# Optimization experiments

Hardware: AMD Instinct MI355X
Metric: run time of the kernel (lower is better)

## Reference

```python
import jax, jax.numpy as jnp
import numpy as np
import math

B, L, D, H = 2, 2048, 1024, 16
DK = D // H  # 64


def _lin(k, din, dout):
    kw, kb = jax.random.split(k)
    w = jax.random.normal(kw, (din, dout), dtype=jnp.float32) * 0.02
    b = jax.random.normal(kb, (dout,), dtype=jnp.float32) * 0.02
    return w, b


def setup_inputs() -> dict:
    key = jax.random.key(0)
    ks = jax.random.split(key, 12)
    wq, bq = _lin(ks[0], D, D)
    wk, bk = _lin(ks[1], D, D)
    wv, bv = _lin(ks[2], D, D)
    wo, bo = _lin(ks[3], D, D)
    whq, bhq = _lin(ks[4], DK, DK)
    whk, bhk = _lin(ks[5], DK, DK)
    whv, bhv = _lin(ks[6], DK, DK)
    who, bho = _lin(ks[7], DK, DK)
    return {
        "q_input": jax.random.normal(ks[8], (B, L, D), dtype=jnp.float32),
        "k_input": jax.random.normal(ks[9], (B, L, D), dtype=jnp.float32),
        "v_input": jax.random.normal(ks[10], (B, L, D), dtype=jnp.float32),
        "mask": jnp.ones((B, 1, L, L), dtype=jnp.int32),
        "wq": wq, "bq": bq, "wk": wk, "bk": bk, "wv": wv, "bv": bv,
        "wo": wo, "bo": bo,
        "whq": whq, "bhq": bhq, "whk": whk, "bhk": bhk,
        "whv": whv, "bhv": bhv, "who": who, "bho": bho,
    }


def reference(q_input, k_input, v_input, mask, wq, bq, wk, bk, wv, bv, wo, bo,
              whq, bhq, whk, bhk, whv, bhv, who, bho):
    scale = 1.0 / math.sqrt(DK)
    # Q/K/V projections -> [B, H, L, DK]
    Q = (q_input @ wq + bq).reshape(B, L, H, DK).transpose(0, 2, 1, 3)
    K = (k_input @ wk + bk).reshape(B, L, H, DK).transpose(0, 2, 1, 3)
    V = (v_input @ wv + bv).reshape(B, L, H, DK).transpose(0, 2, 1, 3)
    scores = jnp.einsum('bhqd,bhkd->bhqk', Q, K) * scale  # [B,H,L,L]
    neg = jnp.finfo(scores.dtype).min
    scores = jnp.where(mask == 0, neg, scores)
    probs = jax.nn.softmax(scores, axis=-1)  # dropout is identity in eval
    attn = jnp.einsum('bhqk,bhkd->bhqd', probs, V)
    heads = attn.transpose(0, 2, 1, 3)  # [B, L, H, DK]
    # Inter-head attention over the head dimension (size H) per position
    Qh = heads @ whq + bhq
    Kh = heads @ whk + bhk
    Vh = heads @ whv + bhv
    inter = jnp.einsum('blhd,blgd->blhg', Qh, Kh) * scale  # [B,L,H,H]
    iprobs = jax.nn.softmax(inter, axis=-1)
    mixed = jnp.einsum('blhg,blgd->blhd', iprobs, Vh)  # [B,L,H,DK]
    # note: inter_head_out is defined but unused in the original forward
    concat = mixed.reshape(B, L, D)
    return concat @ wo + bo
```

## Files before the change

kernel.cpp:

```cpp
#include <hip/hip_runtime.h>
#include <hip/hip_bf16.h>

typedef __bf16 bf16_t;
typedef __bf16 bf16x4 __attribute__((ext_vector_type(4)));
typedef __bf16 bf16x8 __attribute__((ext_vector_type(8)));
typedef float f32x4 __attribute__((ext_vector_type(4)));

typedef __attribute__((address_space(1))) unsigned char glob_u8;
typedef __attribute__((address_space(3))) unsigned char lds_u8;

__device__ __forceinline__ void load_lds16(const void* g, void* l) {
    __builtin_amdgcn_global_load_lds((glob_u8*)g, (lds_u8*)l, 16, 0, 0);
}

__global__ void prep1_kernel(const int* __restrict__ mask, int* __restrict__ flags,
                             const float* __restrict__ wq, const float* __restrict__ wk,
                             const float* __restrict__ wv, bf16_t* __restrict__ wqkvT,
                             const float* __restrict__ aq, const float* __restrict__ ak,
                             const float* __restrict__ av, bf16_t* __restrict__ abf)
{
    const int bid = blockIdx.x, t = threadIdx.x;
    if (bid < 2048) {
        int b = bid >> 10, qt = (bid >> 5) & 31, kt = bid & 31;
        int ok = 1;
#pragma unroll
        for (int i = 0; i < 16; i++) {
            int e = t + i * 256; int r = e >> 6, c = e & 63;
            ok &= (mask[((size_t)b * 2048 + qt * 64 + r) * 2048 + kt * 64 + c] != 0) ? 1 : 0;
        }
        ok = __syncthreads_and(ok);
        if (t == 0) flags[bid] = ok;
    } else if (bid < 2816) {
        __shared__ bf16_t tile[64][65];
        int idx = bid - 2048;
        int z = idx >> 8, rem = idx & 255;
        const float* src = (z == 0) ? wq : (z == 1) ? wk : wv;
        bf16_t* dst = wqkvT + (size_t)z * 1048576;
        int rB = (rem >> 4) * 64, cB = (rem & 15) * 64;
#pragma unroll
        for (int i = 0; i < 16; i++) {
            int e = t + i * 256; int r = e >> 6, c = e & 63;
            tile[r][c] = (bf16_t)src[(size_t)(rB + r) * 1024 + cB + c];
        }
        __syncthreads();
#pragma unroll
        for (int i = 0; i < 16; i++) {
            int e = t + i * 256; int r = e >> 6, c = e & 63;
            dst[(size_t)(cB + r) * 1024 + rB + c] = tile[c][r];
        }
    } else {
        int idx = bid - 2816;
        int z = idx >> 9, seg = idx & 511;
        const float* src = (z == 0) ? aq : (z == 1) ? ak : av;
        bf16_t* dst = abf + (size_t)z * 4194304;
        size_t base = (size_t)seg * 8192 + (size_t)t * 32;
#pragma unroll
        for (int j = 0; j < 4; j++) {
            f32x4 u = *(const f32x4*)(src + base + j * 8);
            f32x4 v = *(const f32x4*)(src + base + j * 8 + 4);
            bf16x8 o;
            o[0] = (bf16_t)u[0]; o[1] = (bf16_t)u[1];
            o[2] = (bf16_t)u[2]; o[3] = (bf16_t)u[3];
            o[4] = (bf16_t)v[0]; o[5] = (bf16_t)v[1];
            o[6] = (bf16_t)v[2]; o[7] = (bf16_t)v[3];
            *(bf16x8*)(dst + base + j * 8) = o;
        }
    }
}

__global__ void prep2_kernel(const float* __restrict__ wo, bf16_t* __restrict__ woT,
                             const float* __restrict__ s0, const float* __restrict__ s1,
                             const float* __restrict__ s2,
                             bf16_t* __restrict__ d0, bf16_t* __restrict__ d1, bf16_t* __restrict__ d2)
{
    const int bid = blockIdx.x, t = threadIdx.x;
    if (bid < 256) {
        __shared__ bf16_t tile[64][65];
        int rB = (bid >> 4) * 64, cB = (bid & 15) * 64;
#pragma unroll
        for (int i = 0; i < 16; i++) {
            int e = t + i * 256; int r = e >> 6, c = e & 63;
            tile[r][c] = (bf16_t)wo[(size_t)(rB + r) * 1024 + cB + c];
        }
        __syncthreads();
#pragma unroll
        for (int i = 0; i < 16; i++) {
            int e = t + i * 256; int r = e >> 6, c = e & 63;
            woT[(size_t)(cB + r) * 1024 + rB + c] = tile[c][r];
        }
    } else {
        int z = bid - 256;
        const float* src = (z == 0) ? s0 : (z == 1) ? s1 : s2;
        bf16_t* dst = (z == 0) ? d0 : (z == 1) ? d1 : d2;
#pragma unroll
        for (int i = 0; i < 16; i++) {
            int e = t + i * 256; int r = e >> 6, c = e & 63;
            dst[c * 64 + r] = (bf16_t)src[r * 64 + c];
        }
    }
}

#define GS 40

template<bool BF16A>
__global__ __launch_bounds__(256, 2) void gemm_qkv_t(
    const float* __restrict__ Aq, const float* __restrict__ Ak, const float* __restrict__ Av,
    const bf16_t* __restrict__ Abf,
    const bf16_t* __restrict__ WT,
    const float* __restrict__ bq, const float* __restrict__ bk, const float* __restrict__ bv,
    bf16_t* __restrict__ outbase)
{
    __shared__ bf16_t As[128 * GS];
    __shared__ bf16_t Bs[128 * GS];
    const int z = blockIdx.z;
    const float* A    = (z == 0) ? Aq : (z == 1) ? Ak : Av;
    const bf16_t* Ab  = Abf + (size_t)z * 4194304;
    const bf16_t* Bt  = WT + (size_t)z * 1048576;
    const float* bia  = (z == 0) ? bq : (z == 1) ? bk : bv;
    bf16_t* out = outbase + (size_t)z * 4194304;

    const int t = threadIdx.x;
    const int w = t >> 6, lane = t & 63;
    const int lane15 = lane & 15, quad = lane >> 4;
    const int wr = w >> 1, wc = w & 1;
    const int rowBase = blockIdx.x * 128, colBase = blockIdx.y * 128;

    const int ar = t >> 1, ac = (t & 1) * 16;
    const int e0 = t * 8, e1 = (256 + t) * 8;
    const int r0 = e0 >> 5, c0 = e0 & 31;
    const int r1 = e1 >> 5, c1 = e1 & 31;

    f32x4 acc[4][4];
    f32x4 zf = {0.f, 0.f, 0.f, 0.f};
#pragma unroll
    for (int i = 0; i < 4; i++)
#pragma unroll
        for (int j = 0; j < 4; j++) acc[i][j] = zf;

    for (int k0 = 0; k0 < 1024; k0 += 32) {
        bf16x8 av0, av1;
        if (BF16A) {
            const bf16_t* ab = Ab + (size_t)(rowBase + ar) * 1024 + k0 + ac;
            av0 = *(const bf16x8*)(ab);
            av1 = *(const bf16x8*)(ab + 8);
        } else {
            const float4* ap = (const float4*)(A + (size_t)(rowBase + ar) * 1024 + k0 + ac);
            float4 af4[4];
#pragma unroll
            for (int i = 0; i < 4; i++) af4[i] = ap[i];
#pragma unroll
            for (int i = 0; i < 4; i++) {
                bf16x8& dstv = (i < 2) ? av0 : av1;
                int base = (i & 1) * 4;
                dstv[base + 0] = (bf16_t)af4[i].x; dstv[base + 1] = (bf16_t)af4[i].y;
                dstv[base + 2] = (bf16_t)af4[i].z; dstv[base + 3] = (bf16_t)af4[i].w;
            }
        }
        bf16x8 b0 = *(const bf16x8*)(Bt + (size_t)(colBase + r0) * 1024 + k0 + c0);
        bf16x8 b1 = *(const bf16x8*)(Bt + (size_t)(colBase + r1) * 1024 + k0 + c1);
        *(bf16x8*)(As + ar * GS + ac) = av0;
        *(bf16x8*)(As + ar * GS + ac + 8) = av1;
        *(bf16x8*)(Bs + r0 * GS + c0) = b0;
        *(bf16x8*)(Bs + r1 * GS + c1) = b1;
        __syncthreads();
        bf16x8 afr[4], bfr[4];
#pragma unroll
        for (int mi = 0; mi < 4; mi++)
            afr[mi] = *(const bf16x8*)(As + (wr * 64 + mi * 16 + lane15) * GS + quad * 8);
#pragma unroll
        for (int ni = 0; ni < 4; ni++)
            bfr[ni] = *(const bf16x8*)(Bs + (wc * 64 + ni * 16 + lane15) * GS + quad * 8);
#pragma unroll
        for (int mi = 0; mi < 4; mi++)
#pragma unroll
            for (int ni = 0; ni < 4; ni++)
                acc[mi][ni] = __builtin_amdgcn_mfma_f32_16x16x32_bf16(afr[mi], bfr[ni], acc[mi][ni], 0, 0, 0);
        __syncthreads();
    }

#pragma unroll
    for (int ni = 0; ni < 4; ni++) {
        int col = colBase + wc * 64 + ni * 16 + lane15;
        float bias = bia[col];
        int h = col >> 6, dk = col & 63;
#pragma unroll
        for (int mi = 0; mi < 4; mi++) {
#pragma unroll
            for (int r = 0; r < 4; r++) {
                int row = rowBase + wr * 64 + mi * 16 + quad * 4 + r;
                int b = row >> 11, l = row & 2047;
                float v = acc[mi][ni][r] + bias;
                size_t dst = (z < 2) ? ((((size_t)(b * 16 + h)) * 2048 + l) * 64 + dk)
                                     : ((((size_t)(b * 16 + h)) * 64 + dk) * 2048 + l);
                out[dst] = (bf16_t)v;
            }
        }
    }
}

__global__ __launch_bounds__(256, 2) void gemm_out_kernel(
    const bf16_t* __restrict__ A, const bf16_t* __restrict__ Bt,
    const float* __restrict__ bia, float* __restrict__ out)
{
    __shared__ bf16_t As[128 * 32];
    __shared__ bf16_t Bs[64 * 32];
    const int t = threadIdx.x;
    const int w = t >> 6, lane = t & 63;
    const int lane15 = lane & 15, quad = lane >> 4;
    const int wr = w >> 1, wc = w & 1;
    const int rowBase = blockIdx.x * 128, colBase = blockIdx.y * 64;

    const int brow = lane >> 2, bcol = (lane & 3) * 8;

    f32x4 acc[4][2];
    f32x4 zf = {0.f, 0.f, 0.f, 0.f};
#pragma unroll
    for (int i = 0; i < 4; i++)
#pragma unroll
        for (int j = 0; j < 2; j++) acc[i][j] = zf;

    for (int k0 = 0; k0 < 1024; k0 += 32) {
#pragma unroll
        for (int j = 0; j < 2; j++) {
            int chunk = w * 2 + j;
            load_lds16(A + (size_t)(rowBase + chunk * 16 + brow) * 1024 + k0 + bcol,
                       (char*)As + chunk * 1024);
        }
        {
            int chunk = w;
            load_lds16(Bt + (size_t)(colBase + chunk * 16 + brow) * 1024 + k0 + bcol,
                       (char*)Bs + chunk * 1024);
        }
        __syncthreads();
        bf16x8 afr[4], bfr[2];
#pragma unroll
        for (int mi = 0; mi < 4; mi++)
            afr[mi] = *(const bf16x8*)(As + (wr * 64 + mi * 16 + lane15) * 32 + quad * 8);
#pragma unroll
        for (int ni = 0; ni < 2; ni++)
            bfr[ni] = *(const bf16x8*)(Bs + (wc * 32 + ni * 16 + lane15) * 32 + quad * 8);
#pragma unroll
        for (int mi = 0; mi < 4; mi++)
#pragma unroll
            for (int ni = 0; ni < 2; ni++)
                acc[mi][ni] = __builtin_amdgcn_mfma_f32_16x16x32_bf16(afr[mi], bfr[ni], acc[mi][ni], 0, 0, 0);
        __syncthreads();
    }

#pragma unroll
    for (int ni = 0; ni < 2; ni++) {
        int col = colBase + wc * 32 + ni * 16 + lane15;
        float bias = bia[col];
#pragma unroll
        for (int mi = 0; mi < 4; mi++) {
#pragma unroll
            for (int r = 0; r < 4; r++) {
                int row = rowBase + wr * 64 + mi * 16 + quad * 4 + r;
                out[(size_t)row * 1024 + col] = acc[mi][ni][r] + bias;
            }
        }
    }
}

#define FS 72

__global__ __launch_bounds__(256, 4) void flash_kernel(
    const bf16_t* __restrict__ QKV, const int* __restrict__ mask,
    const int* __restrict__ flags, bf16_t* __restrict__ attnout)
{
    __shared__ bf16_t Ks[64 * FS];
    __shared__ bf16_t Vs[64 * FS];
    __shared__ bf16_t Ps[8 * 16 * FS];
    const int t = threadIdx.x, w = t >> 6, lane = t & 63;
    const int lane15 = lane & 15, quad = lane >> 4;
    const int qt = blockIdx.y, bh = blockIdx.x;
    const int b = bh >> 4, h = bh & 15;
    const bf16_t* Q  = QKV;
    const bf16_t* K  = QKV + 4194304;
    const bf16_t* Vt = QKV + 8388608;
    const int qrow0 = qt * 128 + w * 32;

    bf16x8 aq[2][2];
#pragma unroll
    for (int qf = 0; qf < 2; qf++) {
        const bf16_t* qb = Q + ((size_t)bh * 2048 + qrow0 + qf * 16 + lane15) * 64;
        aq[qf][0] = *(const bf16x8*)(qb + quad * 8);
        aq[qf][1] = *(const bf16x8*)(qb + 32 + quad * 8);
#pragma unroll
        for (int j = 0; j < 8; j++) {
            aq[qf][0][j] = (bf16_t)((float)aq[qf][0][j] * 0.125f);
            aq[qf][1][j] = (bf16_t)((float)aq[qf][1][j] * 0.125f);
        }
    }

    f32x4 zf = {0.f, 0.f, 0.f, 0.f};
    f32x4 o[2][4];
#pragma unroll
    for (int qf = 0; qf < 2; qf++)
#pragma unroll
        for (int df = 0; df < 4; df++) o[qf][df] = zf;
    f32x4 lsum[2] = {zf, zf};
    bf16_t* Pw0 = Ps + (w * 2 + 0) * 16 * FS;
    bf16_t* Pw1 = Ps + (w * 2 + 1) * 16 * FS;
    bf16x8 ones;
#pragma unroll
    for (int j = 0; j < 8; j++) ones[j] = (bf16_t)1.0f;

    const int e0 = t * 8, e1 = (256 + t) * 8;
    const int kr0 = e0 >> 6, kc0 = e0 & 63, kr1 = e1 >> 6, kc1 = e1 & 63;
    const int* flagrow = flags + (b * 32 + qt) * 32;
    const bf16_t* Kb  = K  + (size_t)bh * 131072;
    const bf16_t* Vtb = Vt + (size_t)bh * 131072;

    {
        bf16x8 k0v = *(const bf16x8*)(Kb  + (size_t)kr0 * 64 + kc0);
        bf16x8 k1v = *(const bf16x8*)(Kb  + (size_t)kr1 * 64 + kc1);
        bf16x8 v0v = *(const bf16x8*)(Vtb + (size_t)kr0 * 2048 + kc0);
        bf16x8 v1v = *(const bf16x8*)(Vtb + (size_t)kr1 * 2048 + kc1);
        *(bf16x8*)(Ks + kr0 * FS + kc0) = k0v;
        *(bf16x8*)(Ks + kr1 * FS + kc1) = k1v;
        *(bf16x8*)(Vs + kr0 * FS + kc0) = v0v;
        *(bf16x8*)(Vs + kr1 * FS + kc1) = v1v;
    }
    __syncthreads();

    for (int kt = 0; kt < 32; kt++) {
        bf16x8 k0v, k1v, v0v, v1v;
        if (kt + 1 < 32) {
            int kn = (kt + 1) * 64;
            k0v = *(const bf16x8*)(Kb  + (size_t)(kn + kr0) * 64 + kc0);
            k1v = *(const bf16x8*)(Kb  + (size_t)(kn + kr1) * 64 + kc1);
            v0v = *(const bf16x8*)(Vtb + (size_t)kr0 * 2048 + kn + kc0);
            v1v = *(const bf16x8*)(Vtb + (size_t)kr1 * 2048 + kn + kc1);
        }

        f32x4 st[2][4];
#pragma unroll
        for (int kf = 0; kf < 4; kf++) {
            bf16x8 kb0 = *(const bf16x8*)(Ks + (kf * 16 + lane15) * FS + quad * 8);
            bf16x8 kb1 = *(const bf16x8*)(Ks + (kf * 16 + lane15) * FS + 32 + quad * 8);
#pragma unroll
            for (int qf = 0; qf < 2; qf++) {
                f32x4 a = zf;
                a = __builtin_amdgcn_mfma_f32_16x16x32_bf16(kb0, aq[qf][0], a, 0, 0, 0);
                a = __builtin_amdgcn_mfma_f32_16x16x32_bf16(kb1, aq[qf][1], a, 0, 0, 0);
                st[qf][kf] = a * 1.44269504f;
            }
        }
        if (!flagrow[kt]) {
#pragma unroll
            for (int qf = 0; qf < 2; qf++)
#pragma unroll
                for (int kf = 0; kf < 4; kf++)
#pragma unroll
                    for (int r = 0; r < 4; r++) {
                        int qrow = qrow0 + qf * 16 + lane15;
                        int kpos = kt * 64 + kf * 16 + quad * 4 + r;
                        if (mask[((size_t)b * 2048 + qrow) * 2048 + kpos] == 0)
                            st[qf][kf][r] = -1e30f;
                    }
        }
#pragma unroll
        for (int qf = 0; qf < 2; qf++) {
            bf16_t* Pq = qf ? Pw1 : Pw0;
#pragma unroll
            for (int kf = 0; kf < 4; kf++) {
                bf16x4 pv;
#pragma unroll
                for (int r = 0; r < 4; r++) pv[r] = (bf16_t)exp2f(st[qf][kf][r]);
                *(bf16x4*)(Pq + lane15 * FS + kf * 16 + quad * 4) = pv;
            }
        }
        bf16x8 pa[2][2];
        pa[0][0] = *(const bf16x8*)(Pw0 + lane15 * FS + quad * 8);
        pa[0][1] = *(const bf16x8*)(Pw0 + lane15 * FS + 32 + quad * 8);
        pa[1][0] = *(const bf16x8*)(Pw1 + lane15 * FS + quad * 8);
        pa[1][1] = *(const bf16x8*)(Pw1 + lane15 * FS + 32 + quad * 8);
#pragma unroll
        for (int qf = 0; qf < 2; qf++) {
            lsum[qf] = __builtin_amdgcn_mfma_f32_16x16x32_bf16(ones, pa[qf][0], lsum[qf], 0, 0, 0);
            lsum[qf] = __builtin_amdgcn_mfma_f32_16x16x32_bf16(ones, pa[qf][1], lsum[qf], 0, 0, 0);
        }
#pragma unroll
        for (int df = 0; df < 4; df++) {
            bf16x8 vb0 = *(const bf16x8*)(Vs + (df * 16 + lane15) * FS + quad * 8);
            bf16x8 vb1 = *(const bf16x8*)(Vs + (df * 16 + lane15) * FS + 32 + quad * 8);
#pragma unroll
            for (int qf = 0; qf < 2; qf++) {
                o[qf][df] = __builtin_amdgcn_mfma_f32_16x16x32_bf16(pa[qf][0], vb0, o[qf][df], 0, 0, 0);
                o[qf][df] = __builtin_amdgcn_mfma_f32_16x16x32_bf16(pa[qf][1], vb1, o[qf][df], 0, 0, 0);
            }
        }

        if (kt + 1 < 32) {
            __syncthreads();
            *(bf16x8*)(Ks + kr0 * FS + kc0) = k0v;
            *(bf16x8*)(Ks + kr1 * FS + kc1) = k1v;
            *(bf16x8*)(Vs + kr0 * FS + kc0) = v0v;
            *(bf16x8*)(Vs + kr1 * FS + kc1) = v1v;
            __syncthreads();
        }
    }

#pragma unroll
    for (int qf = 0; qf < 2; qf++) {
        float lv = lsum[qf][0];
#pragma unroll
        for (int r = 0; r < 4; r++) {
            float inv = 1.0f / __shfl(lv, quad * 4 + r, 64);
            size_t row = (size_t)b * 2048 + qrow0 + qf * 16 + quad * 4 + r;
#pragma unroll
            for (int df = 0; df < 4; df++)
                attnout[(row * 16 + h) * 64 + df * 16 + lane15] = (bf16_t)(o[qf][df][r] * inv);
        }
    }
}

__global__ __launch_bounds__(256, 2) void interhead_kernel(
    const bf16_t* __restrict__ attn,
    const bf16_t* __restrict__ whqT, const float* __restrict__ bhq,
    const bf16_t* __restrict__ whkT, const float* __restrict__ bhk,
    const bf16_t* __restrict__ whvT, const float* __restrict__ bhv,
    bf16_t* __restrict__ concat)
{
    __shared__ bf16_t lds[4 * 4608];
    const int t = threadIdx.x, w = t >> 6, lane = t & 63;
    const int lane15 = lane & 15, quad = lane >> 4;
    bf16_t* Qh  = lds + w * 4608;
    bf16_t* Kh  = Qh + 1024;
    bf16_t* VhT = Kh + 1024;
    bf16_t* P16 = VhT + 2048;
    const int p = blockIdx.x * 4 + w;

    bf16x8 z8 = {(bf16_t)0.f, (bf16_t)0.f, (bf16_t)0.f, (bf16_t)0.f,
                 (bf16_t)0.f, (bf16_t)0.f, (bf16_t)0.f, (bf16_t)0.f};
    ((bf16x8*)P16)[lane] = z8;
#pragma unroll
    for (int i = 0; i < 4; i++) ((bf16x8*)VhT)[i * 64 + lane] = z8;

    const bf16_t* hb = attn + ((size_t)p * 16 + lane15) * 64;
    bf16x8 ha0 = *(const bf16x8*)(hb + quad * 8);
    bf16x8 ha1 = *(const bf16x8*)(hb + 32 + quad * 8);

    const bf16_t* Wt[3] = {whqT, whkT, whvT};
    const float*  Bb[3] = {bhq, bhk, bhv};
    f32x4 zf = {0.f, 0.f, 0.f, 0.f};
#pragma unroll
    for (int m3 = 0; m3 < 3; m3++) {
#pragma unroll
        for (int nf = 0; nf < 4; nf++) {
            f32x4 acc = zf;
            bf16x8 wb0 = *(const bf16x8*)(Wt[m3] + (nf * 16 + lane15) * 64 + quad * 8);
            bf16x8 wb1 = *(const bf16x8*)(Wt[m3] + (nf * 16 + lane15) * 64 + 32 + quad * 8);
            acc = __builtin_amdgcn_mfma_f32_16x16x32_bf16(ha0, wb0, acc, 0, 0, 0);
            acc = __builtin_amdgcn_mfma_f32_16x16x32_bf16(ha1, wb1, acc, 0, 0, 0);
            float bias = Bb[m3][nf * 16 + lane15];
#pragma unroll
            for (int r = 0; r < 4; r++) {
                float v = acc[r] + bias;
                if (m3 == 0) v *= 0.125f;
                if (m3 == 2) VhT[(nf * 16 + lane15) * 32 + quad * 4 + r] = (bf16_t)v;
                else if (m3 == 0) Qh[(quad * 4 + r) * 64 + nf * 16 + lane15] = (bf16_t)v;
                else Kh[(quad * 4 + r) * 64 + nf * 16 + lane15] = (bf16_t)v;
            }
        }
    }
    __syncthreads();

    bf16x8 qa0 = *(const bf16x8*)(Qh + lane15 * 64 + quad * 8);
    bf16x8 qa1 = *(const bf16x8*)(Qh + lane15 * 64 + 32 + quad * 8);
    bf16x8 kb0 = *(const bf16x8*)(Kh + lane15 * 64 + quad * 8);
    bf16x8 kb1 = *(const bf16x8*)(Kh + lane15 * 64 + 32 + quad * 8);
    f32x4 s = zf;
    s = __builtin_amdgcn_mfma_f32_16x16x32_bf16(qa0, kb0, s, 0, 0, 0);
    s = __builtin_amdgcn_mfma_f32_16x16x32_bf16(qa1, kb1, s, 0, 0, 0);
#pragma unroll
    for (int r = 0; r < 4; r++) {
        float v = s[r];
        float mx = v;
        mx = fmaxf(mx, __shfl_xor(mx, 1));
        mx = fmaxf(mx, __shfl_xor(mx, 2));
        mx = fmaxf(mx, __shfl_xor(mx, 4));
        mx = fmaxf(mx, __shfl_xor(mx, 8));
        float pv = __expf(v - mx);
        float sm = pv;
        sm += __shfl_xor(sm, 1);
        sm += __shfl_xor(sm, 2);
        sm += __shfl_xor(sm, 4);
        sm += __shfl_xor(sm, 8);
        P16[(quad * 4 + r) * 32 + lane15] = (bf16_t)(pv / sm);
    }
    __syncthreads();

    bf16x8 pa = *(const bf16x8*)(P16 + lane15 * 32 + quad * 8);
    bf16_t* outp = concat + (size_t)p * 1024;
#pragma unroll
    for (int df = 0; df < 4; df++) {
        bf16x8 vb = *(const bf16x8*)(VhT + (df * 16 + lane15) * 32 + quad * 8);
        f32x4 mix = zf;
        mix = __builtin_amdgcn_mfma_f32_16x16x32_bf16(pa, vb, mix, 0, 0, 0);
#pragma unroll
        for (int r = 0; r < 4; r++)
            outp[(quad * 4 + r) * 64 + df * 16 + lane15] = (bf16_t)mix[r];
    }
}

extern "C" void kernel_launch(void* const* d_in, const int* in_sizes, int n_in,
                              void* d_out, int out_size, void* d_ws, size_t ws_size,
                              hipStream_t stream)
{
    const float* q_in = (const float*)d_in[0];
    const float* k_in = (const float*)d_in[1];
    const float* v_in = (const float*)d_in[2];
    const int*   mask = (const int*)d_in[3];
    const float* wq = (const float*)d_in[4];
    const float* bq = (const float*)d_in[5];
    const float* wk = (const float*)d_in[6];
    const float* bk = (const float*)d_in[7];
    const float* wv = (const float*)d_in[8];
    const float* bv = (const float*)d_in[9];
    const float* wo = (const float*)d_in[10];
    const float* bo = (const float*)d_in[11];
    const float* whq = (const float*)d_in[12];
    const float* bhq = (const float*)d_in[13];
    const float* whk = (const float*)d_in[14];
    const float* bhk = (const float*)d_in[15];
    const float* whv = (const float*)d_in[16];
    const float* bhv = (const float*)d_in[17];
    float* out = (float*)d_out;

    char* ws = (char*)d_ws;
    bf16_t* qkvb  = (bf16_t*)ws;
    bf16_t* concat = qkvb;
    bf16_t* woT   = (bf16_t*)(ws + 8u * 1024 * 1024);
    bf16_t* whqT  = (bf16_t*)(ws + 10u * 1024 * 1024);
    bf16_t* whkT  = whqT + 4096;
    bf16_t* whvT  = whqT + 8192;
    bf16_t* abf   = (bf16_t*)(ws + 24u * 1024 * 1024);
    bf16_t* attnb = (bf16_t*)d_out;
    bf16_t* wqkvT = (bf16_t*)((char*)d_out + 8u * 1024 * 1024);
    int*    flags = (int*)((char*)d_out + 14u * 1024 * 1024);

    const bool bigws = (ws_size >= 48u * 1024 * 1024);

    prep1_kernel<<<bigws ? 4352 : 2816, 256, 0, stream>>>(
        mask, flags, wq, wk, wv, wqkvT, q_in, k_in, v_in, abf);
    if (bigws)
        gemm_qkv_t<true><<<dim3(32, 8, 3), 256, 0, stream>>>(
            q_in, k_in, v_in, abf, wqkvT, bq, bk, bv, qkvb);
    else
        gemm_qkv_t<false><<<dim3(32, 8, 3), 256, 0, stream>>>(
            q_in, k_in, v_in, abf, wqkvT, bq, bk, bv, qkvb);
    flash_kernel<<<dim3(32, 16), 256, 0, stream>>>(qkvb, mask, flags, attnb);
    prep2_kernel<<<259, 256, 0, stream>>>(wo, woT, whq, whk, whv, whqT, whkT, whvT);
    interhead_kernel<<<1024, 256, 0, stream>>>(attnb, whqT, bhq, whkT, bhk, whvT, bhv, concat);
    gemm_out_kernel<<<dim3(32, 16), 256, 0, stream>>>(concat, woT, bo, out);
    (void)in_sizes; (void)n_in; (void)out_size; (void)ws_size;
}
```

Measured before the change: 310.7 us.

## Split flash attention over key range with atomic fp32 partials merged in interhead

```diff
diff --git a/kernel.cpp b/kernel.cpp
--- a/kernel.cpp
+++ b/kernel.cpp
@@ -264,9 +264,11 @@
 
 #define FS 72
 
+template<int NSPLIT>
 __global__ __launch_bounds__(256, 4) void flash_kernel(
     const bf16_t* __restrict__ QKV, const int* __restrict__ mask,
-    const int* __restrict__ flags, bf16_t* __restrict__ attnout)
+    const int* __restrict__ flags, bf16_t* __restrict__ attnout,
+    float* __restrict__ pO, float* __restrict__ pL)
 {
     __shared__ bf16_t Ks[64 * FS];
     __shared__ bf16_t Vs[64 * FS];
@@ -274,6 +276,8 @@
     const int t = threadIdx.x, w = t >> 6, lane = t & 63;
     const int lane15 = lane & 15, quad = lane >> 4;
     const int qt = blockIdx.y, bh = blockIdx.x;
+    const int ks = blockIdx.z;
+    const int kt0 = ks * (32 / NSPLIT), kt1 = kt0 + (32 / NSPLIT);
     const int b = bh >> 4, h = bh & 15;
     const bf16_t* Q  = QKV;
     const bf16_t* K  = QKV + 4194304;
@@ -308,15 +312,17 @@
 
     const int e0 = t * 8, e1 = (256 + t) * 8;
     const int kr0 = e0 >> 6, kc0 = e0 & 63, kr1 = e1 >> 6, kc1 = e1 & 63;
-    const int* flagrow = flags + (b * 32 + qt) * 32;
+    const int* fr0 = flags + (b * 32 + 2 * qt) * 32;
+    const int* fr1 = fr0 + 32;
     const bf16_t* Kb  = K  + (size_t)bh * 131072;
     const bf16_t* Vtb = Vt + (size_t)bh * 131072;
 
     {
-        bf16x8 k0v = *(const bf16x8*)(Kb  + (size_t)kr0 * 64 + kc0);
-        bf16x8 k1v = *(const bf16x8*)(Kb  + (size_t)kr1 * 64 + kc1);
-        bf16x8 v0v = *(const bf16x8*)(Vtb + (size_t)kr0 * 2048 + kc0);
-        bf16x8 v1v = *(const bf16x8*)(Vtb + (size_t)kr1 * 2048 + kc1);
+        int kn0 = kt0 * 64;
+        bf16x8 k0v = *(const bf16x8*)(Kb  + (size_t)(kn0 + kr0) * 64 + kc0);
+        bf16x8 k1v = *(const bf16x8*)(Kb  + (size_t)(kn0 + kr1) * 64 + kc1);
+        bf16x8 v0v = *(const bf16x8*)(Vtb + (size_t)kr0 * 2048 + kn0 + kc0);
+        bf16x8 v1v = *(const bf16x8*)(Vtb + (size_t)kr1 * 2048 + kn0 + kc1);
         *(bf16x8*)(Ks + kr0 * FS + kc0) = k0v;
         *(bf16x8*)(Ks + kr1 * FS + kc1) = k1v;
         *(bf16x8*)(Vs + kr0 * FS + kc0) = v0v;
@@ -324,9 +330,9 @@
     }
     __syncthreads();
 
-    for (int kt = 0; kt < 32; kt++) {
+    for (int kt = kt0; kt < kt1; kt++) {
         bf16x8 k0v, k1v, v0v, v1v;
-        if (kt + 1 < 32) {
+        if (kt + 1 < kt1) {
             int kn = (kt + 1) * 64;
             k0v = *(const bf16x8*)(Kb  + (size_t)(kn + kr0) * 64 + kc0);
             k1v = *(const bf16x8*)(Kb  + (size_t)(kn + kr1) * 64 + kc1);
@@ -347,7 +353,7 @@
                 st[qf][kf] = a * 1.44269504f;
             }
         }
-        if (!flagrow[kt]) {
+        if (!(fr0[kt] & fr1[kt])) {
 #pragma unroll
             for (int qf = 0; qf < 2; qf++)
 #pragma unroll
@@ -392,7 +398,7 @@
             }
         }
 
-        if (kt + 1 < 32) {
+        if (kt + 1 < kt1) {
             __syncthreads();
             *(bf16x8*)(Ks + kr0 * FS + kc0) = k0v;
             *(bf16x8*)(Ks + kr1 * FS + kc1) = k1v;
@@ -402,22 +408,42 @@
         }
     }
 
-#pragma unroll
-    for (int qf = 0; qf < 2; qf++) {
-        float lv = lsum[qf][0];
-#pragma unroll
-        for (int r = 0; r < 4; r++) {
-            float inv = 1.0f / __shfl(lv, quad * 4 + r, 64);
-            size_t row = (size_t)b * 2048 + qrow0 + qf * 16 + quad * 4 + r;
+    if (NSPLIT == 1) {
+#pragma unroll
+        for (int qf = 0; qf < 2; qf++) {
+            float lv = lsum[qf][0];
+#pragma unroll
+            for (int r = 0; r < 4; r++) {
+                float inv = 1.0f / __shfl(lv, quad * 4 + r, 64);
+                size_t row = (size_t)b * 2048 + qrow0 + qf * 16 + quad * 4 + r;
+#pragma unroll
+                for (int df = 0; df < 4; df++)
+                    attnout[(row * 16 + h) * 64 + df * 16 + lane15] = (bf16_t)(o[qf][df][r] * inv);
+            }
+        }
+    } else {
+#pragma unroll
+        for (int qf = 0; qf < 2; qf++) {
+            if (lane < 16) {
+                size_t l = (size_t)qrow0 + qf * 16 + lane;
+                atomicAdd(&pL[((size_t)b * 2048 + l) * 16 + h], lsum[qf][0]);
+            }
 #pragma unroll
             for (int df = 0; df < 4; df++)
-                attnout[(row * 16 + h) * 64 + df * 16 + lane15] = (bf16_t)(o[qf][df][r] * inv);
-        }
-    }
-}
-
+#pragma unroll
+                for (int r = 0; r < 4; r++) {
+                    size_t l = (size_t)qrow0 + qf * 16 + quad * 4 + r;
+                    atomicAdd(&pO[(((size_t)b * 2048 + l) * 16 + h) * 64 + df * 16 + lane15],
+                              o[qf][df][r]);
+                }
+        }
+    }
+}
+
+template<bool F32IN>
 __global__ __launch_bounds__(256, 2) void interhead_kernel(
     const bf16_t* __restrict__ attn,
+    const float* __restrict__ pO, const float* __restrict__ pL,
     const bf16_t* __restrict__ whqT, const float* __restrict__ bhq,
     const bf16_t* __restrict__ whkT, const float* __restrict__ bhk,
     const bf16_t* __restrict__ whvT, const float* __restrict__ bhv,
@@ -438,9 +464,27 @@
 #pragma unroll
     for (int i = 0; i < 4; i++) ((bf16x8*)VhT)[i * 64 + lane] = z8;
 
-    const bf16_t* hb = attn + ((size_t)p * 16 + lane15) * 64;
-    bf16x8 ha0 = *(const bf16x8*)(hb + quad * 8);
-    bf16x8 ha1 = *(const bf16x8*)(hb + 32 + quad * 8);
+    bf16x8 ha0, ha1;
+    if (F32IN) {
+        size_t r16 = (size_t)p * 16 + lane15;
+        float inv = 1.0f / pL[r16];
+        const float* src = pO + r16 * 64;
+        f32x4 u0 = *(const f32x4*)(src + quad * 8);
+        f32x4 u1 = *(const f32x4*)(src + quad * 8 + 4);
+        f32x4 u2 = *(const f32x4*)(src + 32 + quad * 8);
+        f32x4 u3 = *(const f32x4*)(src + 32 + quad * 8 + 4);
+#pragma unroll
+        for (int j = 0; j < 4; j++) {
+            ha0[j]     = (bf16_t)(u0[j] * inv);
+            ha0[j + 4] = (bf16_t)(u1[j] * inv);
+            ha1[j]     = (bf16_t)(u2[j] * inv);
+            ha1[j + 4] = (bf16_t)(u3[j] * inv);
+        }
+    } else {
+        const bf16_t* hb = attn + ((size_t)p * 16 + lane15) * 64;
+        ha0 = *(const bf16x8*)(hb + quad * 8);
+        ha1 = *(const bf16x8*)(hb + 32 + quad * 8);
+    }
 
     const bf16_t* Wt[3] = {whqT, whkT, whvT};
     const float*  Bb[3] = {bhq, bhk, bhv};
@@ -537,6 +581,8 @@
     bf16_t* whkT  = whqT + 4096;
     bf16_t* whvT  = whqT + 8192;
     bf16_t* abf   = (bf16_t*)(ws + 24u * 1024 * 1024);
+    float*  pO    = (float*)(ws + 24u * 1024 * 1024);
+    float*  pL    = pO + (size_t)4096 * 16 * 64;
     bf16_t* attnb = (bf16_t*)d_out;
     bf16_t* wqkvT = (bf16_t*)((char*)d_out + 8u * 1024 * 1024);
     int*    flags = (int*)((char*)d_out + 14u * 1024 * 1024);
@@ -551,9 +597,21 @@
     else
         gemm_qkv_t<false><<<dim3(32, 8, 3), 256, 0, stream>>>(
             q_in, k_in, v_in, abf, wqkvT, bq, bk, bv, qkvb);
-    flash_kernel<<<dim3(32, 16), 256, 0, stream>>>(qkvb, mask, flags, attnb);
+    if (bigws) {
+        hipMemsetAsync(pO, 0, (size_t)4096 * 16 * 64 * 4 + (size_t)4096 * 16 * 4, stream);
+        flash_kernel<2><<<dim3(32, 16, 2), 256, 0, stream>>>(
+            qkvb, mask, flags, attnb, pO, pL);
+    } else {
+        flash_kernel<1><<<dim3(32, 16, 1), 256, 0, stream>>>(
+            qkvb, mask, flags, attnb, pO, pL);
+    }
     prep2_kernel<<<259, 256, 0, stream>>>(wo, woT, whq, whk, whv, whqT, whkT, whvT);
-    interhead_kernel<<<1024, 256, 0, stream>>>(attnb, whqT, bhq, whkT, bhk, whvT, bhv, concat);
+    if (bigws)
+        interhead_kernel<true><<<1024, 256, 0, stream>>>(
+            attnb, pO, pL, whqT, bhq, whkT, bhk, whvT, bhv, concat);
+    else
+        interhead_kernel<false><<<1024, 256, 0, stream>>>(
+            attnb, pO, pL, whqT, bhq, whkT, bhk, whvT, bhv, concat);
     gemm_out_kernel<<<dim3(32, 16), 256, 0, stream>>>(concat, woT, bo, out);
     (void)in_sizes; (void)n_in; (void)out_size; (void)ws_size;
 }
```

After: 326.1 us. +5.0%, slower.
